# Kernel tuning notes

Measured on AMD Instinct MI355X. Metric: run time of the kernel, lower is better.

Reference implementation:

```python
import jax, jax.numpy as jnp
import numpy as np

N, Lq, Lk, D = 4, 2048, 2048, 1024
H, DH = 16, 64  # n_heads, projection_dim
NEG_INF = jnp.float32(-1e30)


def setup_inputs() -> dict:
    key = jax.random.key(0)
    ks = jax.random.split(key, 6)
    query = jax.random.normal(ks[0], (N, Lq, D), dtype=jnp.float32)
    key_t = jax.random.normal(ks[1], (N, Lk, D), dtype=jnp.float32)
    s = 1.0 / np.sqrt(D)
    Wq = jax.random.normal(ks[2], (D, D), dtype=jnp.float32) * s
    Wk = jax.random.normal(ks[3], (D, D), dtype=jnp.float32) * s
    Wv = jax.random.normal(ks[4], (D, D), dtype=jnp.float32) * s
    # causal mask: True where attention is forbidden (j > i)
    mask = jnp.triu(jnp.ones((Lq, Lk), dtype=bool), k=1)
    # per-sample valid lengths in [1024, 2048); padding at the tail
    valid_len = jax.random.randint(ks[5], (N,), Lk // 2, Lk)
    padding_mask = jnp.arange(Lk)[None, :] >= valid_len[:, None]  # (N, Lk) bool
    return {"query": query, "key": key_t, "Wq": Wq, "Wk": Wk, "Wv": Wv,
            "mask": mask, "padding_mask": padding_mask}


def reference(query, key, Wq, Wk, Wv, mask, padding_mask):
    n, lq, _ = query.shape
    lk = key.shape[1]
    # torch Linear (no bias): x @ W.T ; split heads -> (N, H, L, DH)
    q = (query @ Wq.T).reshape(n, lq, H, DH).transpose(0, 2, 1, 3)
    k = (key @ Wk.T).reshape(n, lk, H, DH).transpose(0, 2, 1, 3)
    v = (key @ Wv.T).reshape(n, lk, H, DH).transpose(0, 2, 1, 3)
    # per-sample scaling: sqrt(number of non-padded keys) (module quirk, not sqrt(d))
    valid = jnp.sum(~padding_mask, axis=-1).astype(query.dtype)  # (N,)
    scaling = jnp.sqrt(valid)[:, None, None, None]
    score = jnp.einsum('nhqd,nhkd->nhqk', q, k) / scaling
    score = jnp.where(mask[None, None, :, :], NEG_INF, score)
    score = jnp.where(padding_mask[:, None, None, :], NEG_INF, score)
    attn = jax.nn.softmax(score, axis=-1)
    out = jnp.einsum('nhqk,nhkd->nhqd', attn, v)
    return out.transpose(0, 2, 1, 3).reshape(n, lq, H * DH)
```

## Files before the change

### kernel.cpp

```cpp
#include <hip/hip_runtime.h>
#include <hip/hip_bf16.h>
#include <math.h>


#define N_S 4
#define LQ 2048
#define LK 2048
#define DM 1024
#define NHEAD 16
#define DHEAD 64

typedef __attribute__((ext_vector_type(8))) short short8;
typedef __attribute__((ext_vector_type(4))) float f32x4;

typedef const __attribute__((address_space(1))) void* gptr_t;
typedef __attribute__((address_space(3))) void* lptr_t;

#define GLOAD_LDS(g, l) \
    __builtin_amdgcn_global_load_lds((gptr_t)(const void*)(g), (lptr_t)(void*)(l), 16, 0, 0)

static __device__ __forceinline__ unsigned int pkbf(float a, float b) {
    __hip_bfloat162 h = __float22bfloat162_rn(make_float2(a, b));
    unsigned int u;
    __builtin_memcpy(&u, &h, 4);
    return u;
}

static __device__ __forceinline__ f32x4 zero4() {
    f32x4 v; v[0] = 0.f; v[1] = 0.f; v[2] = 0.f; v[3] = 0.f; return v;
}

static __device__ __forceinline__ void meta_body(const void* __restrict__ pm,
                                                 int* __restrict__ valid_out,
                                                 float* __restrict__ scale_out) {
    __shared__ int okInt, hasPair, okF32;
    __shared__ int counts[4];
    int t = threadIdx.x;
    if (t == 0) { okInt = 1; hasPair = 0; okF32 = 1; }
    if (t < 4) counts[t] = 0;
    __syncthreads();

    const unsigned int* w = (const unsigned int*)pm;
    int bad_int = 0, pair = 0, bad_f32 = 0;
    for (int i = t; i < 2048; i += 256) {
        unsigned int v = w[i];
        if (v > 1u) bad_int = 1;
        if (v == 0x3F803F80u) pair = 1;
        if (v != 0u && v != 0x3F800000u) bad_f32 = 1;
    }
    if (bad_int) okInt = 0;
    if (pair)    hasPair = 1;
    if (bad_f32) okF32 = 0;
    __syncthreads();

    int mode = okInt ? 0 : (hasPair ? 1 : (okF32 ? 2 : 3));
    for (int n = 0; n < 4; n++) {
        int cnt = 0;
        for (int j = t; j < LK; j += 256) {
            int idx = n * LK + j;
            bool z;
            if (mode == 0)      z = (((const int*)pm)[idx] == 0);
            else if (mode == 1) z = (((const unsigned short*)pm)[idx] == 0);
            else if (mode == 2) z = (w[idx] == 0u);
            else                z = (((const unsigned char*)pm)[idx] == 0);
            cnt += z ? 1 : 0;
        }
        atomicAdd(&counts[n], cnt);
    }
    __syncthreads();
    if (t < 4) {
        int c = counts[t] > 0 ? counts[t] : 1;
        valid_out[t] = c;
        scale_out[t] = 1.0f / sqrtf((float)c);
    }
}

__global__ void meta_kernel(const void* __restrict__ pm,
                            int* __restrict__ valid_out,
                            float* __restrict__ scale_out) {
    meta_body(pm, valid_out, scale_out);
}

static __device__ __forceinline__ void conv16(const float* src,
                                              unsigned short* dst, size_t idx) {
    f32x4 a0 = *(const f32x4*)(src + idx);
    f32x4 a1 = *(const f32x4*)(src + idx + 4);
    f32x4 a2 = *(const f32x4*)(src + idx + 8);
    f32x4 a3 = *(const f32x4*)(src + idx + 12);
    uint4 u0, u1;
    u0.x = pkbf(a0[0], a0[1]); u0.y = pkbf(a0[2], a0[3]);
    u0.z = pkbf(a1[0], a1[1]); u0.w = pkbf(a1[2], a1[3]);
    u1.x = pkbf(a2[0], a2[1]); u1.y = pkbf(a2[2], a2[3]);
    u1.z = pkbf(a3[0], a3[1]); u1.w = pkbf(a3[2], a3[3]);
    *(uint4*)(void*)(dst + idx) = u0;
    *(uint4*)(void*)(dst + idx + 8) = u1;
}

__global__ __launch_bounds__(256) void convw_kernel(
    const float* __restrict__ Wq, const float* __restrict__ Wk,
    const float* __restrict__ Wv,
    unsigned short* __restrict__ Wqb, unsigned short* __restrict__ Wkb,
    unsigned short* __restrict__ Wvb)
{
    int z = blockIdx.y;
    const float* src = (z == 0) ? Wq : ((z == 1) ? Wk : Wv);
    unsigned short* dst = (z == 0) ? Wqb : ((z == 1) ? Wkb : Wvb);
    conv16(src, dst, ((size_t)blockIdx.x * 256 + threadIdx.x) * 16);
}

__global__ __launch_bounds__(256) void convx_kernel(
    const float* __restrict__ src, unsigned short* __restrict__ dst)
{
    conv16(src, dst, ((size_t)blockIdx.x * 256 + threadIdx.x) * 16);
}

__global__ __launch_bounds__(256) void prep_kernel(
    const void* __restrict__ pm, int* __restrict__ valid_out,
    float* __restrict__ scale_out,
    const float* __restrict__ Wq, const float* __restrict__ Wk,
    const float* __restrict__ Wv,
    unsigned short* __restrict__ Wqb, unsigned short* __restrict__ Wkb,
    unsigned short* __restrict__ Wvb,
    const float* __restrict__ xq, const float* __restrict__ xk,
    unsigned short* __restrict__ dq, unsigned short* __restrict__ dk)
{
    int b = blockIdx.x;
    int t = threadIdx.x;
    if (b == 0) {
        meta_body(pm, valid_out, scale_out);
    } else if (b <= 768) {
        int bb = b - 1;
        int z = bb >> 8;
        const float* src = (z == 0) ? Wq : ((z == 1) ? Wk : Wv);
        unsigned short* dst = (z == 0) ? Wqb : ((z == 1) ? Wkb : Wvb);
        conv16(src, dst, ((size_t)(bb & 255) * 256 + t) * 16);
    } else {
        int bb = b - 769;
        const float* src = (bb >= 2048) ? xk : xq;
        unsigned short* dst = (bb >= 2048) ? dk : dq;
        int x = (bb >= 2048) ? bb - 2048 : bb;
        conv16(src, dst, ((size_t)x * 256 + t) * 16);
    }
}

__global__ __launch_bounds__(256) void proj_bf16_kernel(
    const unsigned short* __restrict__ XbQ, const unsigned short* __restrict__ XbK,
    const unsigned short* __restrict__ Wqb, const unsigned short* __restrict__ Wkb,
    const unsigned short* __restrict__ Wvb,
    const float* __restrict__ scal,
    unsigned short* __restrict__ Qb, unsigned short* __restrict__ Kb,
    unsigned short* __restrict__ Vt, int zbase)
{
    int z = blockIdx.z + zbase;
    const unsigned short* W = (z == 0) ? Wqb : ((z == 1) ? Wkb : Wvb);
    const unsigned short* Xb = (z == 0) ? XbQ : XbK;

    __shared__ unsigned short Xls[128 * 32];
    __shared__ unsigned short Wls[128 * 32];

    int t = threadIdx.x;
    int wave = t >> 6, lane = t & 63;
    int l15 = lane & 15, quad = lane >> 4;
    int wa = wave >> 1, wb = wave & 1;
    int m0 = blockIdx.x << 7, n0 = blockIdx.y << 7;

    int srow = t >> 2;
    int sg = ((t & 3) ^ (srow & 3)) << 3;
    const unsigned short* gX0 = Xb + (size_t)(m0 + srow) * DM + sg;
    const unsigned short* gX1 = Xb + (size_t)(m0 + 64 + srow) * DM + sg;
    const unsigned short* gW0 = W + (size_t)(n0 + srow) * DM + sg;
    const unsigned short* gW1 = W + (size_t)(n0 + 64 + srow) * DM + sg;

    f32x4 acc[4][4];
    #pragma unroll
    for (int i = 0; i < 4; i++)
        #pragma unroll
        for (int j = 0; j < 4; j++) acc[i][j] = zero4();

    int aoff = ((quad ^ (l15 & 3)) << 3);
    const unsigned short* Abuf = (z < 2) ? Wls : Xls;
    const unsigned short* Bbuf = (z < 2) ? Xls : Wls;

    for (int kk = 0; kk < DM; kk += 32) {
        __syncthreads();
        GLOAD_LDS(gX0 + kk, Xls + wave * 512);
        GLOAD_LDS(gX1 + kk, Xls + 2048 + wave * 512);
        GLOAD_LDS(gW0 + kk, Wls + wave * 512);
        GLOAD_LDS(gW1 + kk, Wls + 2048 + wave * 512);
        __syncthreads();

        short8 af[4], bf[4];
        #pragma unroll
        for (int ai = 0; ai < 4; ai++)
            af[ai] = *(const short8*)(const void*)(
                Abuf + ((wa * 64 + ai * 16 + l15) << 5) + aoff);
        #pragma unroll
        for (int bi = 0; bi < 4; bi++)
            bf[bi] = *(const short8*)(const void*)(
                Bbuf + ((wb * 64 + bi * 16 + l15) << 5) + aoff);
        #pragma unroll
        for (int ai = 0; ai < 4; ai++)
            #pragma unroll
            for (int bi = 0; bi < 4; bi++)
                acc[ai][bi] = __builtin_amdgcn_mfma_f32_16x16x32_bf16(
                    af[ai], bf[bi], acc[ai][bi], 0, 0, 0);
    }

    if (z < 2) {
        unsigned short* O = (z == 0) ? Qb : Kb;
        #pragma unroll
        for (int bi = 0; bi < 4; bi++) {
            int token = m0 + wb * 64 + bi * 16 + l15;
            float qs = 1.0f;
            if (z == 0) qs = scal[token >> 11] * 1.44269504f;
            #pragma unroll
            for (int ai = 0; ai < 4; ai++) {
                int feat = n0 + wa * 64 + ai * 16 + quad * 4;
                float v0 = acc[ai][bi][0], v1 = acc[ai][bi][1];
                float v2 = acc[ai][bi][2], v3 = acc[ai][bi][3];
                if (z == 0) { v0 *= qs; v1 *= qs; v2 *= qs; v3 *= qs; }
                uint2 u;
                u.x = pkbf(v0, v1);
                u.y = pkbf(v2, v3);
                *(uint2*)(void*)(O + (size_t)token * DM + feat) = u;
            }
        }
    } else {
        #pragma unroll
        for (int ai = 0; ai < 4; ai++) {
            int token0 = m0 + wa * 64 + ai * 16 + quad * 4;
            int n = token0 >> 11, tl = token0 & 2047;
            #pragma unroll
            for (int bi = 0; bi < 4; bi++) {
                int feat = n0 + wb * 64 + bi * 16 + l15;
                uint2 u;
                u.x = pkbf(acc[ai][bi][0], acc[ai][bi][1]);
                u.y = pkbf(acc[ai][bi][2], acc[ai][bi][3]);
                *(uint2*)(void*)(Vt + ((size_t)n * DM + feat) * LK + tl) = u;
            }
        }
    }
}

__global__ __launch_bounds__(256) void proj_f32_kernel(
    const float* __restrict__ Xq, const float* __restrict__ Xk,
    const unsigned short* __restrict__ Wqb, const unsigned short* __restrict__ Wkb,
    const unsigned short* __restrict__ Wvb,
    const float* __restrict__ scal,
    unsigned short* __restrict__ Qb, unsigned short* __restrict__ Kb,
    unsigned short* __restrict__ Vt)
{
    int z = blockIdx.z;
    const float* X = (z == 0) ? Xq : Xk;
    const unsigned short* W = (z == 0) ? Wqb : ((z == 1) ? Wkb : Wvb);

    __shared__ unsigned short Xls[128 * 32];
    __shared__ unsigned short Wls[128 * 32];

    int t = threadIdx.x;
    int wave = t >> 6, lane = t & 63;
    int l15 = lane & 15, quad = lane >> 4;
    int wa = wave >> 1, wb = wave & 1;
    int m0 = blockIdx.x << 7, n0 = blockIdx.y << 7;

    int arow = t >> 1, ah = t & 1;
    int ag0 = ((2 * ah)     ^ (arow & 3)) << 3;
    int ag1 = ((2 * ah + 1) ^ (arow & 3)) << 3;
    const float* gX = X + (size_t)(m0 + arow) * DM;
    unsigned short* lX = Xls + arow * 32 + ah * 16;

    int brow = t >> 2;
    int bg = ((t & 3) ^ (brow & 3)) << 3;
    const unsigned short* gW0 = W + (size_t)(n0 + brow) * DM + bg;
    const unsigned short* gW1 = W + (size_t)(n0 + 64 + brow) * DM + bg;

    f32x4 acc[4][4];
    #pragma unroll
    for (int i = 0; i < 4; i++)
        #pragma unroll
        for (int j = 0; j < 4; j++) acc[i][j] = zero4();

    int aoff = ((quad ^ (l15 & 3)) << 3);

    f32x4 an0 = *(const f32x4*)(gX + ag0);
    f32x4 an1 = *(const f32x4*)(gX + ag0 + 4);
    f32x4 an2 = *(const f32x4*)(gX + ag1);
    f32x4 an3 = *(const f32x4*)(gX + ag1 + 4);

    const unsigned short* Abuf = (z < 2) ? Wls : Xls;
    const unsigned short* Bbuf = (z < 2) ? Xls : Wls;

    for (int kk = 0; kk < DM; kk += 32) {
        __syncthreads();
        GLOAD_LDS(gW0 + kk, Wls + wave * 512);
        GLOAD_LDS(gW1 + kk, Wls + 2048 + wave * 512);
        uint4 ua, ub;
        ua.x = pkbf(an0[0], an0[1]); ua.y = pkbf(an0[2], an0[3]);
        ua.z = pkbf(an1[0], an1[1]); ua.w = pkbf(an1[2], an1[3]);
        ub.x = pkbf(an2[0], an2[1]); ub.y = pkbf(an2[2], an2[3]);
        ub.z = pkbf(an3[0], an3[1]); ub.w = pkbf(an3[2], an3[3]);
        *(uint4*)(void*)(lX)     = ua;
        *(uint4*)(void*)(lX + 8) = ub;
        __syncthreads();

        if (kk + 32 < DM) {
            an0 = *(const f32x4*)(gX + kk + 32 + ag0);
            an1 = *(const f32x4*)(gX + kk + 32 + ag0 + 4);
            an2 = *(const f32x4*)(gX + kk + 32 + ag1);
            an3 = *(const f32x4*)(gX + kk + 32 + ag1 + 4);
        }

        short8 af[4], bf[4];
        #pragma unroll
        for (int ai = 0; ai < 4; ai++)
            af[ai] = *(const short8*)(const void*)(
                Abuf + ((wa * 64 + ai * 16 + l15) << 5) + aoff);
        #pragma unroll
        for (int bi = 0; bi < 4; bi++)
            bf[bi] = *(const short8*)(const void*)(
                Bbuf + ((wb * 64 + bi * 16 + l15) << 5) + aoff);
        #pragma unroll
        for (int ai = 0; ai < 4; ai++)
            #pragma unroll
            for (int bi = 0; bi < 4; bi++)
                acc[ai][bi] = __builtin_amdgcn_mfma_f32_16x16x32_bf16(
                    af[ai], bf[bi], acc[ai][bi], 0, 0, 0);
    }

    if (z < 2) {
        unsigned short* O = (z == 0) ? Qb : Kb;
        #pragma unroll
        for (int bi = 0; bi < 4; bi++) {
            int token = m0 + wb * 64 + bi * 16 + l15;
            float qs = 1.0f;
            if (z == 0) qs = scal[token >> 11] * 1.44269504f;
            #pragma unroll
            for (int ai = 0; ai < 4; ai++) {
                int feat = n0 + wa * 64 + ai * 16 + quad * 4;
                float v0 = acc[ai][bi][0], v1 = acc[ai][bi][1];
                float v2 = acc[ai][bi][2], v3 = acc[ai][bi][3];
                if (z == 0) { v0 *= qs; v1 *= qs; v2 *= qs; v3 *= qs; }
                uint2 u;
                u.x = pkbf(v0, v1);
                u.y = pkbf(v2, v3);
                *(uint2*)(void*)(O + (size_t)token * DM + feat) = u;
            }
        }
    } else {
        #pragma unroll
        for (int ai = 0; ai < 4; ai++) {
            int token0 = m0 + wa * 64 + ai * 16 + quad * 4;
            int n = token0 >> 11, tl = token0 & 2047;
            #pragma unroll
            for (int bi = 0; bi < 4; bi++) {
                int feat = n0 + wb * 64 + bi * 16 + l15;
                uint2 u;
                u.x = pkbf(acc[ai][bi][0], acc[ai][bi][1]);
                u.y = pkbf(acc[ai][bi][2], acc[ai][bi][3]);
                *(uint2*)(void*)(Vt + ((size_t)n * DM + feat) * LK + tl) = u;
            }
        }
    }
}

__global__ __launch_bounds__(256) void attn_kernel(
    const unsigned short* __restrict__ Qb, const unsigned short* __restrict__ Kb,
    const unsigned short* __restrict__ Vt,
    const int* __restrict__ valid_arr,
    float* __restrict__ out)
{
    __shared__ unsigned short Kls[3][64 * 64];

    int bx = blockIdx.x;
    int nh = blockIdx.y;
    int n = nh >> 4, h = nh & 15;
    int tA = bx, tB = 31 - bx;

    int valid = valid_arr[n];
    int tvalid = (valid + 63) >> 6;
    int TlA = (tA + 1 < tvalid) ? tA + 1 : tvalid;
    int TlB = (tB + 1 < tvalid) ? tB + 1 : tvalid;

    int t = threadIdx.x;
    int wave = t >> 6, lane = t & 63;
    int l15 = lane & 15, quad = lane >> 4;

    int qyA = tA * 64 + wave * 16 + l15;
    int qyB = tB * 64 + wave * 16 + l15;
    int qw0A = tA * 64 + wave * 16;
    int qw0B = tB * 64 + wave * 16;

    const unsigned short* QrowA = Qb + ((size_t)n * LQ + qyA) * DM + h * DHEAD;
    const unsigned short* QrowB = Qb + ((size_t)n * LQ + qyB) * DM + h * DHEAD;
    short8 qfA0 = *(const short8*)(const void*)(QrowA + quad * 8);
    short8 qfA1 = *(const short8*)(const void*)(QrowA + 32 + quad * 8);
    short8 qfB0 = *(const short8*)(const void*)(QrowB + quad * 8);
    short8 qfB1 = *(const short8*)(const void*)(QrowB + 32 + quad * 8);

    f32x4 OA[4], OB[4];
    #pragma unroll
    for (int i = 0; i < 4; i++) { OA[i] = zero4(); OB[i] = zero4(); }
    f32x4 LAcc = zero4(), LBcc = zero4();

    short8 onesf;
    #pragma unroll
    for (int i = 0; i < 8; i++) onesf[i] = (short)0x3F80;

    const unsigned short* Kbase = Kb + (size_t)n * LK * DM + h * DHEAD;
    const unsigned short* Vbase = Vt + ((size_t)n * DM + h * DHEAD) * LK;

    int srow0 = t >> 3;
    int sgk   = (((t & 7) ^ (srow0 & 7)) << 3);

    GLOAD_LDS(Kbase + (size_t)srow0 * DM + sgk,        &Kls[0][0] + wave * 512);
    GLOAD_LDS(Kbase + (size_t)(32 + srow0) * DM + sgk, &Kls[0][0] + 2048 + wave * 512);
    if (TlB > 1) {
        GLOAD_LDS(Kbase + (size_t)(64 + srow0) * DM + sgk,
                  &Kls[1][0] + wave * 512);
        GLOAD_LDS(Kbase + (size_t)(96 + srow0) * DM + sgk,
                  &Kls[1][0] + 2048 + wave * 512);
        asm volatile("s_waitcnt vmcnt(2)" ::: "memory");
    } else {
        asm volatile("s_waitcnt vmcnt(0)" ::: "memory");
    }

    int cur = 0;
    for (int kt = 0; kt < TlB; kt++) {
        int jb = kt << 6;
        bool doA = (kt < TlA);
        int nxt = (cur == 0) ? 2 : cur - 1;

        __builtin_amdgcn_sched_barrier(0);
        __builtin_amdgcn_s_barrier();
        __builtin_amdgcn_sched_barrier(0);

        f32x4 sA[4], sB[4];
        __builtin_amdgcn_s_setprio(1);
        #pragma unroll
        for (int cb = 0; cb < 4; cb++) {
            const unsigned short* krow = &Kls[cur][0] + ((cb * 16 + l15) << 6);
            short8 kf0 = *(const short8*)(const void*)(krow + ((quad ^ (l15 & 7)) << 3));
            short8 kf1 = *(const short8*)(const void*)(krow + (((4 + quad) ^ (l15 & 7)) << 3));
            f32x4 sb = zero4();
            sb = __builtin_amdgcn_mfma_f32_16x16x32_bf16(kf0, qfB0, sb, 0, 0, 0);
            sb = __builtin_amdgcn_mfma_f32_16x16x32_bf16(kf1, qfB1, sb, 0, 0, 0);
            sB[cb] = sb;
            if (doA) {
                f32x4 sa = zero4();
                sa = __builtin_amdgcn_mfma_f32_16x16x32_bf16(kf0, qfA0, sa, 0, 0, 0);
                sa = __builtin_amdgcn_mfma_f32_16x16x32_bf16(kf1, qfA1, sa, 0, 0, 0);
                sA[cb] = sa;
            }
        }
        __builtin_amdgcn_s_setprio(0);

        short8 vf0[4], vf1[4];
        #pragma unroll
        for (int cb = 0; cb < 4; cb++) {
            vf0[cb] = *(const short8*)(const void*)(
                Vbase + (size_t)(cb * 16 + l15) * LK + jb + quad * 8);
            vf1[cb] = *(const short8*)(const void*)(
                Vbase + (size_t)(cb * 16 + l15) * LK + jb + 32 + quad * 8);
        }
        if (kt + 2 < TlB) {
            int jb2 = jb + 128;
            GLOAD_LDS(Kbase + (size_t)(jb2 + srow0) * DM + sgk,
                      &Kls[nxt][0] + wave * 512);
            GLOAD_LDS(Kbase + (size_t)(jb2 + 32 + srow0) * DM + sgk,
                      &Kls[nxt][0] + 2048 + wave * 512);
        }

        if (jb + 63 > qw0B || jb + 64 > valid) {
            #pragma unroll
            for (int cb = 0; cb < 4; cb++) {
                int jb2 = jb + cb * 16 + quad * 4;
                #pragma unroll
                for (int r = 0; r < 4; r++) {
                    int j = jb2 + r;
                    if (j > qyB || j >= valid) sB[cb][r] = -1e30f;
                }
            }
        }
        short8 pfB0, pfB1;
        {
            unsigned int lo[4], hi[4];
            #pragma unroll
            for (int cb = 0; cb < 4; cb++) {
                lo[cb] = pkbf(__builtin_amdgcn_exp2f(sB[cb][0]),
                              __builtin_amdgcn_exp2f(sB[cb][1]));
                hi[cb] = pkbf(__builtin_amdgcn_exp2f(sB[cb][2]),
                              __builtin_amdgcn_exp2f(sB[cb][3]));
            }
            asm("v_permlane32_swap_b32 %0, %1" : "+v"(lo[0]), "+v"(lo[1]));
            asm("v_permlane32_swap_b32 %0, %1" : "+v"(hi[0]), "+v"(hi[1]));
            asm("v_permlane32_swap_b32 %0, %1" : "+v"(lo[2]), "+v"(lo[3]));
            asm("v_permlane32_swap_b32 %0, %1" : "+v"(hi[2]), "+v"(hi[3]));
            asm("v_permlane16_swap_b32 %0, %1" : "+v"(lo[0]), "+v"(lo[1]));
            asm("v_permlane16_swap_b32 %0, %1" : "+v"(hi[0]), "+v"(hi[1]));
            asm("v_permlane16_swap_b32 %0, %1" : "+v"(lo[2]), "+v"(lo[3]));
            asm("v_permlane16_swap_b32 %0, %1" : "+v"(hi[2]), "+v"(hi[3]));
            uint4 w0, w1;
            w0.x = lo[0]; w0.y = hi[0]; w0.z = lo[1]; w0.w = hi[1];
            w1.x = lo[2]; w1.y = hi[2]; w1.z = lo[3]; w1.w = hi[3];
            __builtin_memcpy(&pfB0, &w0, 16);
            __builtin_memcpy(&pfB1, &w1, 16);
        }

        __builtin_amdgcn_s_setprio(1);
        #pragma unroll
        for (int cb = 0; cb < 4; cb++) {
            OB[cb] = __builtin_amdgcn_mfma_f32_16x16x32_bf16(pfB0, vf0[cb], OB[cb], 0, 0, 0);
            OB[cb] = __builtin_amdgcn_mfma_f32_16x16x32_bf16(pfB1, vf1[cb], OB[cb], 0, 0, 0);
        }
        LBcc = __builtin_amdgcn_mfma_f32_16x16x32_bf16(pfB0, onesf, LBcc, 0, 0, 0);
        LBcc = __builtin_amdgcn_mfma_f32_16x16x32_bf16(pfB1, onesf, LBcc, 0, 0, 0);
        __builtin_amdgcn_s_setprio(0);

        if (doA) {
            if (jb + 63 > qw0A || jb + 64 > valid) {
                #pragma unroll
                for (int cb = 0; cb < 4; cb++) {
                    int jb2 = jb + cb * 16 + quad * 4;
                    #pragma unroll
                    for (int r = 0; r < 4; r++) {
                        int j = jb2 + r;
                        if (j > qyA || j >= valid) sA[cb][r] = -1e30f;
                    }
                }
            }
            short8 pfA0, pfA1;
            {
                unsigned int lo[4], hi[4];
                #pragma unroll
                for (int cb = 0; cb < 4; cb++) {
                    lo[cb] = pkbf(__builtin_amdgcn_exp2f(sA[cb][0]),
                                  __builtin_amdgcn_exp2f(sA[cb][1]));
                    hi[cb] = pkbf(__builtin_amdgcn_exp2f(sA[cb][2]),
                                  __builtin_amdgcn_exp2f(sA[cb][3]));
                }
                asm("v_permlane32_swap_b32 %0, %1" : "+v"(lo[0]), "+v"(lo[1]));
                asm("v_permlane32_swap_b32 %0, %1" : "+v"(hi[0]), "+v"(hi[1]));
                asm("v_permlane32_swap_b32 %0, %1" : "+v"(lo[2]), "+v"(lo[3]));
                asm("v_permlane32_swap_b32 %0, %1" : "+v"(hi[2]), "+v"(hi[3]));
                asm("v_permlane16_swap_b32 %0, %1" : "+v"(lo[0]), "+v"(lo[1]));
                asm("v_permlane16_swap_b32 %0, %1" : "+v"(hi[0]), "+v"(hi[1]));
                asm("v_permlane16_swap_b32 %0, %1" : "+v"(lo[2]), "+v"(lo[3]));
                asm("v_permlane16_swap_b32 %0, %1" : "+v"(hi[2]), "+v"(hi[3]));
                uint4 w0, w1;
                w0.x = lo[0]; w0.y = hi[0]; w0.z = lo[1]; w0.w = hi[1];
                w1.x = lo[2]; w1.y = hi[2]; w1.z = lo[3]; w1.w = hi[3];
                __builtin_memcpy(&pfA0, &w0, 16);
                __builtin_memcpy(&pfA1, &w1, 16);
            }
            __builtin_amdgcn_s_setprio(1);
            #pragma unroll
            for (int cb = 0; cb < 4; cb++) {
                OA[cb] = __builtin_amdgcn_mfma_f32_16x16x32_bf16(pfA0, vf0[cb], OA[cb], 0, 0, 0);
                OA[cb] = __builtin_amdgcn_mfma_f32_16x16x32_bf16(pfA1, vf1[cb], OA[cb], 0, 0, 0);
            }
            LAcc = __builtin_amdgcn_mfma_f32_16x16x32_bf16(pfA0, onesf, LAcc, 0, 0, 0);
            LAcc = __builtin_amdgcn_mfma_f32_16x16x32_bf16(pfA1, onesf, LAcc, 0, 0, 0);
            __builtin_amdgcn_s_setprio(0);
        }

        cur = (cur == 2) ? 0 : cur + 1;
    }

    float* obase = out + ((size_t)n * LQ) * DM + h * DHEAD;
    #pragma unroll
    for (int r = 0; r < 4; r++) {
        float iA = 1.0f / LAcc[r];
        float iB = 1.0f / LBcc[r];
        int rowA = tA * 64 + wave * 16 + quad * 4 + r;
        int rowB = tB * 64 + wave * 16 + quad * 4 + r;
        #pragma unroll
        for (int cb = 0; cb < 4; cb++) {
            obase[(size_t)rowA * DM + cb * 16 + l15] = OA[cb][r] * iA;
            obase[(size_t)rowB * DM + cb * 16 + l15] = OB[cb][r] * iB;
        }
    }
}

extern "C" void kernel_launch(void* const* d_in, const int* in_sizes, int n_in,
                              void* d_out, int out_size, void* d_ws, size_t ws_size,
                              hipStream_t stream)
{
    (void)in_sizes; (void)n_in; (void)out_size;

    const float* query = (const float*)d_in[0];
    const float* key   = (const float*)d_in[1];
    const float* Wq    = (const float*)d_in[2];
    const float* Wk    = (const float*)d_in[3];
    const float* Wv    = (const float*)d_in[4];
    const void* pmask  = d_in[6];

    char* ws = (char*)d_ws;
    unsigned short* Qb  = (unsigned short*)(ws);
    unsigned short* Kb  = (unsigned short*)(ws + (size_t)16 * 1024 * 1024);
    unsigned short* Vt  = (unsigned short*)(ws + (size_t)32 * 1024 * 1024);
    int*   valid = (int*)  (ws + (size_t)48 * 1024 * 1024);
    float* scal  = (float*)(ws + (size_t)48 * 1024 * 1024 + 64);
    unsigned short* Wqb = (unsigned short*)(ws + (size_t)48 * 1024 * 1024 + 4096);
    unsigned short* Wkb = Wqb + (size_t)DM * DM;
    unsigned short* Wvb = Wkb + (size_t)DM * DM;
    unsigned short* XbQ = Wvb + (size_t)DM * DM;
    unsigned short* XbK = XbQ + (size_t)N_S * LQ * DM;

    size_t xbytes      = (size_t)N_S * LQ * DM * 2;
    size_t need_phased = (size_t)(48 * 1024 * 1024) + 4096
                       + 3 * (size_t)DM * DM * 2 + xbytes;
    size_t need_full   = need_phased + xbytes;

    if (ws_size >= need_full) {
        prep_kernel<<<dim3(1 + 768 + 4096), 256, 0, stream>>>(
            pmask, valid, scal, Wq, Wk, Wv, Wqb, Wkb, Wvb,
            query, key, XbQ, XbK);
        proj_bf16_kernel<<<dim3(64, 8, 3), 256, 0, stream>>>(
            XbQ, XbK, Wqb, Wkb, Wvb, scal, Qb, Kb, Vt, 0);
    } else if (ws_size >= need_phased) {
        meta_kernel<<<1, 256, 0, stream>>>(pmask, valid, scal);
        convw_kernel<<<dim3(256, 3), 256, 0, stream>>>(Wq, Wk, Wv, Wqb, Wkb, Wvb);
        convx_kernel<<<2048, 256, 0, stream>>>(query, XbQ);
        proj_bf16_kernel<<<dim3(64, 8, 1), 256, 0, stream>>>(
            XbQ, XbQ, Wqb, Wkb, Wvb, scal, Qb, Kb, Vt, 0);
        convx_kernel<<<2048, 256, 0, stream>>>(key, XbQ);
        proj_bf16_kernel<<<dim3(64, 8, 2), 256, 0, stream>>>(
            XbQ, XbQ, Wqb, Wkb, Wvb, scal, Qb, Kb, Vt, 1);
    } else {
        meta_kernel<<<1, 256, 0, stream>>>(pmask, valid, scal);
        convw_kernel<<<dim3(256, 3), 256, 0, stream>>>(Wq, Wk, Wv, Wqb, Wkb, Wvb);
        proj_f32_kernel<<<dim3(64, 8, 3), 256, 0, stream>>>(
            query, key, Wqb, Wkb, Wvb, scal, Qb, Kb, Vt);
    }

    attn_kernel<<<dim3(16, 64), 256, 0, stream>>>(Qb, Kb, Vt, valid,
                                                  (float*)d_out);
}
```

Measured before the change: 331.6 us.

## Skip padded K/V projection tiles, remap block order for XCD locality, hoist V loads

The projection kernel now exits early for K and V row tiles that lie entirely past the valid key length, so padded rows are never computed. The projection and attention launches become 1D grids whose block index is remapped so neighbouring work (same head or same row tile) lands on the same XCD, aiming for better L2 reuse. In the attention loop the V fragment global loads are issued before the QK MFMAs so their latency overlaps the compute. Risks: skipped tiles leave K/Vt rows uninitialised, which relies on attention never reading beyond the valid length, and the earlier V loads raise register pressure.

```diff
diff --git a/kernel.cpp b/kernel.cpp
--- a/kernel.cpp
+++ b/kernel.cpp
@@ -143,15 +143,21 @@
     }
 }
 
-__global__ __launch_bounds__(256) void proj_bf16_kernel(
+static __device__ __forceinline__ void proj_body(
     const unsigned short* __restrict__ XbQ, const unsigned short* __restrict__ XbK,
     const unsigned short* __restrict__ Wqb, const unsigned short* __restrict__ Wkb,
     const unsigned short* __restrict__ Wvb,
-    const float* __restrict__ scal,
+    const float* __restrict__ scal, const int* __restrict__ valid_arr,
     unsigned short* __restrict__ Qb, unsigned short* __restrict__ Kb,
-    unsigned short* __restrict__ Vt, int zbase)
-{
-    int z = blockIdx.z + zbase;
+    unsigned short* __restrict__ Vt, int bxi, int byi, int z)
+{
+    int m0 = bxi << 7, n0 = byi << 7;
+    if (z >= 1) {
+        int n = m0 >> 11, ml = m0 & 2047;
+        int tv64 = ((valid_arr[n] + 63) >> 6) << 6;
+        if (ml >= tv64) return;
+    }
+
     const unsigned short* W = (z == 0) ? Wqb : ((z == 1) ? Wkb : Wvb);
     const unsigned short* Xb = (z == 0) ? XbQ : XbK;
 
@@ -162,7 +168,6 @@
     int wave = t >> 6, lane = t & 63;
     int l15 = lane & 15, quad = lane >> 4;
     int wa = wave >> 1, wb = wave & 1;
-    int m0 = blockIdx.x << 7, n0 = blockIdx.y << 7;
 
     int srow = t >> 2;
     int sg = ((t & 3) ^ (srow & 3)) << 3;
@@ -240,6 +245,34 @@
             }
         }
     }
+}
+
+__global__ __launch_bounds__(256) void proj_bf16_kernel(
+    const unsigned short* __restrict__ XbQ, const unsigned short* __restrict__ XbK,
+    const unsigned short* __restrict__ Wqb, const unsigned short* __restrict__ Wkb,
+    const unsigned short* __restrict__ Wvb,
+    const float* __restrict__ scal, const int* __restrict__ valid_arr,
+    unsigned short* __restrict__ Qb, unsigned short* __restrict__ Kb,
+    unsigned short* __restrict__ Vt, int zbase)
+{
+    proj_body(XbQ, XbK, Wqb, Wkb, Wvb, scal, valid_arr, Qb, Kb, Vt,
+              blockIdx.x, blockIdx.y, blockIdx.z + zbase);
+}
+
+__global__ __launch_bounds__(256) void proj_bf16_swz_kernel(
+    const unsigned short* __restrict__ XbQ, const unsigned short* __restrict__ XbK,
+    const unsigned short* __restrict__ Wqb, const unsigned short* __restrict__ Wkb,
+    const unsigned short* __restrict__ Wvb,
+    const float* __restrict__ scal, const int* __restrict__ valid_arr,
+    unsigned short* __restrict__ Qb, unsigned short* __restrict__ Kb,
+    unsigned short* __restrict__ Vt)
+{
+    int id = blockIdx.x;
+    int s = id >> 3;
+    int g = (id & 7) * 24 + (s >> 3);
+    int y = s & 7;
+    int z = g >> 6, x = g & 63;
+    proj_body(XbQ, XbK, Wqb, Wkb, Wvb, scal, valid_arr, Qb, Kb, Vt, x, y, z);
 }
 
 __global__ __launch_bounds__(256) void proj_f32_kernel(
@@ -371,8 +404,11 @@
 {
     __shared__ unsigned short Kls[3][64 * 64];
 
-    int bx = blockIdx.x;
-    int nh = blockIdx.y;
+    int id = blockIdx.x;
+    int slot = id >> 3;
+    int nh = (id & 7) * 8 + (slot >> 4);
+    int bx = slot & 15;
+
     int n = nh >> 4, h = nh & 15;
     int tA = bx, tB = 31 - bx;
 
@@ -433,6 +469,15 @@
         __builtin_amdgcn_sched_barrier(0);
         __builtin_amdgcn_s_barrier();
         __builtin_amdgcn_sched_barrier(0);
+
+        short8 vf0[4], vf1[4];
+        #pragma unroll
+        for (int cb = 0; cb < 4; cb++) {
+            vf0[cb] = *(const short8*)(const void*)(
+                Vbase + (size_t)(cb * 16 + l15) * LK + jb + quad * 8);
+            vf1[cb] = *(const short8*)(const void*)(
+                Vbase + (size_t)(cb * 16 + l15) * LK + jb + 32 + quad * 8);
+        }
 
         f32x4 sA[4], sB[4];
         __builtin_amdgcn_s_setprio(1);
@@ -454,14 +499,6 @@
         }
         __builtin_amdgcn_s_setprio(0);
 
-        short8 vf0[4], vf1[4];
-        #pragma unroll
-        for (int cb = 0; cb < 4; cb++) {
-            vf0[cb] = *(const short8*)(const void*)(
-                Vbase + (size_t)(cb * 16 + l15) * LK + jb + quad * 8);
-            vf1[cb] = *(const short8*)(const void*)(
-                Vbase + (size_t)(cb * 16 + l15) * LK + jb + 32 + quad * 8);
-        }
         if (kt + 2 < TlB) {
             int jb2 = jb + 128;
             GLOAD_LDS(Kbase + (size_t)(jb2 + srow0) * DM + sgk,
@@ -615,17 +652,17 @@
         prep_kernel<<<dim3(1 + 768 + 4096), 256, 0, stream>>>(
             pmask, valid, scal, Wq, Wk, Wv, Wqb, Wkb, Wvb,
             query, key, XbQ, XbK);
-        proj_bf16_kernel<<<dim3(64, 8, 3), 256, 0, stream>>>(
-            XbQ, XbK, Wqb, Wkb, Wvb, scal, Qb, Kb, Vt, 0);
+        proj_bf16_swz_kernel<<<dim3(1536), 256, 0, stream>>>(
+            XbQ, XbK, Wqb, Wkb, Wvb, scal, valid, Qb, Kb, Vt);
     } else if (ws_size >= need_phased) {
         meta_kernel<<<1, 256, 0, stream>>>(pmask, valid, scal);
         convw_kernel<<<dim3(256, 3), 256, 0, stream>>>(Wq, Wk, Wv, Wqb, Wkb, Wvb);
         convx_kernel<<<2048, 256, 0, stream>>>(query, XbQ);
         proj_bf16_kernel<<<dim3(64, 8, 1), 256, 0, stream>>>(
-            XbQ, XbQ, Wqb, Wkb, Wvb, scal, Qb, Kb, Vt, 0);
+            XbQ, XbQ, Wqb, Wkb, Wvb, scal, valid, Qb, Kb, Vt, 0);
         convx_kernel<<<2048, 256, 0, stream>>>(key, XbQ);
         proj_bf16_kernel<<<dim3(64, 8, 2), 256, 0, stream>>>(
-            XbQ, XbQ, Wqb, Wkb, Wvb, scal, Qb, Kb, Vt, 1);
+            XbQ, XbQ, Wqb, Wkb, Wvb, scal, valid, Qb, Kb, Vt, 1);
     } else {
         meta_kernel<<<1, 256, 0, stream>>>(pmask, valid, scal);
         convw_kernel<<<dim3(256, 3), 256, 0, stream>>>(Wq, Wk, Wv, Wqb, Wkb, Wvb);
@@ -633,6 +670,6 @@
             query, key, Wqb, Wkb, Wvb, scal, Qb, Kb, Vt);
     }
 
-    attn_kernel<<<dim3(16, 64), 256, 0, stream>>>(Qb, Kb, Vt, valid,
-                                                  (float*)d_out);
-}
+    attn_kernel<<<dim3(1024), 256, 0, stream>>>(Qb, Kb, Vt, valid,
+                                                (float*)d_out);
+}
```

Result: no change. 334.2 us (+0.8%).
